# Optimization experiments

Measured on AMD Instinct MI355X. Metric: run time of the kernel, lower is better.

## Reference

```python
import jax, jax.numpy as jnp
import numpy as np

N_VALUES = 10
STRIDE = 2

# sign binarization with straight-through estimator (identity gradient)
@jax.custom_vjp
def binarize(x):
    return jnp.sign(x)

def _bin_fwd(x):
    return jnp.sign(x), None

def _bin_bwd(res, g):
    return (g,)

binarize.defvjp(_bin_fwd, _bin_bwd)


def setup_inputs() -> dict:
    key = jax.random.key(0)
    k1, k2, k3, k4 = jax.random.split(key, 4)
    B, C, H = 16, 1, 28
    D = 2048
    x = jax.random.uniform(k1, (B, C, H, H), dtype=jnp.float32)          # float image in [0,1)
    values = jax.random.normal(k2, (N_VALUES, D), dtype=jnp.float32)     # value-vector embedding table
    w = jax.random.normal(k3, (D, D, 5, 5), dtype=jnp.float32) * 0.05    # binary conv weight (OIHW)
    b = jax.random.normal(k4, (D,), dtype=jnp.float32) * 0.01            # conv bias
    return {"x": x, "values": values, "w": w, "b": b}


def reference(x, values, w, b):
    n = values.shape[0]
    # quantize pixel intensities to value-vector indices (truncation, like .long())
    idx = (x[:, 0] * (n - 1)).astype(jnp.int32)            # [B, H, W]
    # embedding lookup of binarized value vectors
    emb = binarize(values)[idx]                            # [B, H, W, D]
    emb = jnp.transpose(emb, (0, 3, 1, 2))                 # [B, D, H, W]
    # binary-weight conv2d, kernel 5, stride 2, no padding
    out = jax.lax.conv_general_dilated(
        emb, binarize(w),
        window_strides=(STRIDE, STRIDE), padding='VALID',
        dimension_numbers=('NCHW', 'OIHW', 'NCHW'))
    out = out + b[None, :, None, None]                     # [B, D, 12, 12]
    return binarize(out)
```

## Files before the change

### kernel.cpp

```cpp
#include <hip/hip_runtime.h>

#define NV    10
#define DD    2048
#define TAPS  25
#define CHUNK 128
#define NCHH  8
#define NGRP  (DD / 64)
#define HGRP  16
#define OB    64

typedef __attribute__((address_space(1))) const unsigned int gu32;
typedef __attribute__((address_space(3))) unsigned int lu32;

__device__ __forceinline__ float bsign(float v) {
    return (v > 0.0f) ? 1.0f : ((v < 0.0f) ? -1.0f : 0.0f);
}

__global__ __launch_bounds__(64) void vpack_kernel(
        const float* __restrict__ values,
        unsigned long long* __restrict__ vnz,
        unsigned long long* __restrict__ vng) {
    const int b    = blockIdx.x;
    const int n    = b >> 5;
    const int g    = b & 31;
    const int lane = threadIdx.x;
    float f = values[n * DD + g * 64 + lane];
    unsigned long long nz = __ballot(f != 0.0f);
    unsigned long long ng = __ballot(f < 0.0f);
    if (lane == 0) {
        vnz[n * NGRP + g] = nz;
        vng[n * NGRP + g] = ng;
    }
}

__global__ __launch_bounds__(256) void g_kernel(
        const float* __restrict__ w,
        const unsigned long long* __restrict__ gvnz,
        const unsigned long long* __restrict__ gvng,
        float* __restrict__ G) {
    const int bid  = blockIdx.x;
    const int o    = bid >> 1;
    const int half = bid & 1;
    const int t    = threadIdx.x;
    const int lane = t & 63;
    const int wv   = t >> 6;

    __shared__ float ls_raw[CHUNK * TAPS + 32];
    __shared__ unsigned long long s_wnz[2][TAPS * 2];
    __shared__ unsigned long long s_wng[2][TAPS * 2];
    __shared__ unsigned long long s_vnz[NV * HGRP];
    __shared__ unsigned long long s_vng[NV * HGRP];

    const float* wo = w + (size_t)o * (DD * TAPS) + (size_t)half * (1024 * TAPS);

    #define PACK_CHUNK(bi)                                                        \
    {                                                                             \
        _Pragma("unroll")                                                         \
        for (int i = 0; i < 4; ++i) {                                             \
            const int tk = wv + 4 * i;                                            \
            if (tk < 14) {                                                        \
                const int q  = tk >> 1;                                           \
                const int sb = tk & 1;                                            \
                const int t0 = 4 * q;                                             \
                const int ba = (sb * 64 + lane) * TAPS + t0;                      \
                float a0 = ls_raw[ba + 0];                                        \
                float a1 = ls_raw[ba + 1];                                        \
                float a2 = ls_raw[ba + 2];                                        \
                float a3 = ls_raw[ba + 3];                                        \
                unsigned long long z0 = __ballot(a0 != 0.0f);                     \
                unsigned long long g0 = __ballot(a0 <  0.0f);                     \
                unsigned long long z1 = __ballot(a1 != 0.0f);                     \
                unsigned long long g1 = __ballot(a1 <  0.0f);                     \
                unsigned long long z2 = __ballot(a2 != 0.0f);                     \
                unsigned long long g2 = __ballot(a2 <  0.0f);                     \
                unsigned long long z3 = __ballot(a3 != 0.0f);                     \
                unsigned long long g3 = __ballot(a3 <  0.0f);                     \
                if (lane == 0) {                                                  \
                    s_wnz[bi][(t0 + 0) * 2 + sb] = z0;                            \
                    s_wng[bi][(t0 + 0) * 2 + sb] = g0;                            \
                    if (t0 + 1 < TAPS) {                                          \
                        s_wnz[bi][(t0 + 1) * 2 + sb] = z1;                        \
                        s_wng[bi][(t0 + 1) * 2 + sb] = g1;                        \
                        s_wnz[bi][(t0 + 2) * 2 + sb] = z2;                        \
                        s_wng[bi][(t0 + 2) * 2 + sb] = g2;                        \
                        s_wnz[bi][(t0 + 3) * 2 + sb] = z3;                        \
                        s_wng[bi][(t0 + 3) * 2 + sb] = g3;                        \
                    }                                                             \
                }                                                                 \
            }                                                                     \
        }                                                                         \
    }

    for (int e = t; e < (CHUNK * TAPS) / 4; e += 256) {
        __builtin_amdgcn_global_load_lds((gu32*)(wo + 4 * e),
                                         (lu32*)(ls_raw + 4 * (e - lane)), 16, 0, 0);
    }
    if (t < NV * HGRP) {
        const int n  = t >> 4;
        const int gl = t & 15;
        s_vnz[t] = gvnz[n * NGRP + half * HGRP + gl];
        s_vng[t] = gvng[n * NGRP + half * HGRP + gl];
    }
    __syncthreads();
    PACK_CHUNK(0)
    __syncthreads();

    const int tap = t / NV;
    const int n   = t - tap * NV;
    int acc = 0;

    for (int ch = 1; ch <= NCHH; ++ch) {
        if (ch < NCHH) {
            const float* src = wo + (size_t)(ch * CHUNK) * TAPS;
            for (int e = t; e < (CHUNK * TAPS) / 4; e += 256) {
                __builtin_amdgcn_global_load_lds((gu32*)(src + 4 * e),
                                                 (lu32*)(ls_raw + 4 * (e - lane)), 16, 0, 0);
            }
        }
        if (t < NV * TAPS) {
            const int pb = (ch - 1) & 1;
            #pragma unroll
            for (int sub = 0; sub < 2; ++sub) {
                unsigned long long wnz = s_wnz[pb][tap * 2 + sub];
                unsigned long long wng = s_wng[pb][tap * 2 + sub];
                unsigned long long vz  = s_vnz[n * HGRP + (ch - 1) * 2 + sub];
                unsigned long long vg  = s_vng[n * HGRP + (ch - 1) * 2 + sub];
                unsigned long long nzb = wnz & vz;
                acc += (int)__popcll(nzb) - 2 * (int)__popcll((wng ^ vg) & nzb);
            }
        }
        if (ch < NCHH) {
            __syncthreads();
            PACK_CHUNK(ch & 1)
            __syncthreads();
        }
    }
    #undef PACK_CHUNK

    if (t < NV * TAPS) {
        G[((size_t)(half * (TAPS * NV) + tap * NV + n) << 11) + o] = (float)acc;
    }
}

__global__ __launch_bounds__(256) void out_kernel(
        const float* __restrict__ x,
        const float* __restrict__ G,
        const float* __restrict__ bias,
        float* __restrict__ out) {
    const int b     = blockIdx.x >> 5;
    const int oc    = blockIdx.x & 31;
    const int obase = oc * OB;
    const int t     = threadIdx.x;
    const int lane  = t & 63;
    const int oq    = t >> 6;

    __shared__ float s_G[TAPS * NV * 65];
    __shared__ int   s_idx[28 * 28];
    __shared__ float s_bias[OB];

    for (int e = t; e < TAPS * NV * 16; e += 256) {
        const int r  = e >> 4;
        const int li = (e & 15) << 2;
        const float4 va = *(const float4*)(G + ((size_t)r << 11) + obase + li);
        const float4 vb = *(const float4*)(G + ((size_t)(r + TAPS * NV) << 11) + obase + li);
        s_G[r * 65 + li]     = va.x + vb.x;
        s_G[r * 65 + li + 1] = va.y + vb.y;
        s_G[r * 65 + li + 2] = va.z + vb.z;
        s_G[r * 65 + li + 3] = va.w + vb.w;
    }
    for (int e = t; e < 28 * 28; e += 256) {
        s_idx[e] = (int)(x[b * 784 + e] * 9.0f);
    }
    if (t < OB) s_bias[t] = bias[obase + t];
    __syncthreads();

    for (int grp = 0; grp < 3; ++grp) {
        const int pos = grp * 64 + lane;
        if (pos < 144) {
            const int oh = pos / 12;
            const int ow = pos - oh * 12;
            int rr[25];
            #pragma unroll
            for (int kh = 0; kh < 5; ++kh) {
                const int row = (oh * 2 + kh) * 28 + ow * 2;
                #pragma unroll
                for (int kw = 0; kw < 5; ++kw) {
                    const int nn = s_idx[row + kw];
                    rr[kh * 5 + kw] = (kh * 5 + kw) * 650 + nn * 65;
                }
            }
            for (int ol = oq; ol < OB; ol += 4) {
                float acc = 0.0f;
                #pragma unroll
                for (int tp = 0; tp < TAPS; ++tp) {
                    acc += s_G[rr[tp] + ol];
                }
                out[((size_t)(b * DD + obase + ol)) * 144 + pos] = bsign(acc + s_bias[ol]);
            }
        }
    }
}

extern "C" void kernel_launch(void* const* d_in, const int* in_sizes, int n_in,
                              void* d_out, int out_size, void* d_ws, size_t ws_size,
                              hipStream_t stream) {
    const float* x      = (const float*)d_in[0];
    const float* values = (const float*)d_in[1];
    const float* w      = (const float*)d_in[2];
    const float* bias   = (const float*)d_in[3];
    float* out = (float*)d_out;

    unsigned long long* vnz = (unsigned long long*)d_ws;
    unsigned long long* vng = vnz + NV * NGRP;
    float* G = (float*)((char*)d_ws + 8192);

    hipLaunchKernelGGL(vpack_kernel, dim3(NV * NGRP), dim3(64), 0, stream, values, vnz, vng);
    hipLaunchKernelGGL(g_kernel, dim3(2 * DD), dim3(256), 0, stream, w, vnz, vng, G);
    hipLaunchKernelGGL(out_kernel, dim3(16 * (DD / OB)), dim3(256), 0, stream, x, G, bias, out);
}
```

Baseline: 117.2 us.

## Fuse value-bit packing into g_kernel and halve output-channel block size

```diff
diff --git a/kernel.cpp b/kernel.cpp
--- a/kernel.cpp
+++ b/kernel.cpp
@@ -7,7 +7,7 @@
 #define NCHH  8
 #define NGRP  (DD / 64)
 #define HGRP  16
-#define OB    64
+#define OB    32
 
 typedef __attribute__((address_space(1))) const unsigned int gu32;
 typedef __attribute__((address_space(3))) unsigned int lu32;
@@ -16,27 +16,9 @@
     return (v > 0.0f) ? 1.0f : ((v < 0.0f) ? -1.0f : 0.0f);
 }
 
-__global__ __launch_bounds__(64) void vpack_kernel(
+__global__ __launch_bounds__(256) void g_kernel(
         const float* __restrict__ values,
-        unsigned long long* __restrict__ vnz,
-        unsigned long long* __restrict__ vng) {
-    const int b    = blockIdx.x;
-    const int n    = b >> 5;
-    const int g    = b & 31;
-    const int lane = threadIdx.x;
-    float f = values[n * DD + g * 64 + lane];
-    unsigned long long nz = __ballot(f != 0.0f);
-    unsigned long long ng = __ballot(f < 0.0f);
-    if (lane == 0) {
-        vnz[n * NGRP + g] = nz;
-        vng[n * NGRP + g] = ng;
-    }
-}
-
-__global__ __launch_bounds__(256) void g_kernel(
         const float* __restrict__ w,
-        const unsigned long long* __restrict__ gvnz,
-        const unsigned long long* __restrict__ gvng,
         float* __restrict__ G) {
     const int bid  = blockIdx.x;
     const int o    = bid >> 1;
@@ -96,10 +78,24 @@
                                          (lu32*)(ls_raw + 4 * (e - lane)), 16, 0, 0);
     }
     if (t < NV * HGRP) {
-        const int n  = t >> 4;
-        const int gl = t & 15;
-        s_vnz[t] = gvnz[n * NGRP + half * HGRP + gl];
-        s_vng[t] = gvng[n * NGRP + half * HGRP + gl];
+        const int n  = t / HGRP;
+        const int gl = t - n * HGRP;
+        const float4* vp = (const float4*)(values + n * DD + half * 1024 + gl * 64);
+        unsigned long long nz = 0ull, ng = 0ull;
+        #pragma unroll
+        for (int j = 0; j < 16; ++j) {
+            const float4 v = vp[j];
+            if (v.x != 0.0f) nz |= 1ull << (4 * j + 0);
+            if (v.x <  0.0f) ng |= 1ull << (4 * j + 0);
+            if (v.y != 0.0f) nz |= 1ull << (4 * j + 1);
+            if (v.y <  0.0f) ng |= 1ull << (4 * j + 1);
+            if (v.z != 0.0f) nz |= 1ull << (4 * j + 2);
+            if (v.z <  0.0f) ng |= 1ull << (4 * j + 2);
+            if (v.w != 0.0f) nz |= 1ull << (4 * j + 3);
+            if (v.w <  0.0f) ng |= 1ull << (4 * j + 3);
+        }
+        s_vnz[n * HGRP + gl] = nz;
+        s_vng[n * HGRP + gl] = ng;
     }
     __syncthreads();
     PACK_CHUNK(0)
@@ -147,26 +143,26 @@
         const float* __restrict__ G,
         const float* __restrict__ bias,
         float* __restrict__ out) {
-    const int b     = blockIdx.x >> 5;
-    const int oc    = blockIdx.x & 31;
+    const int b     = blockIdx.x >> 6;
+    const int oc    = blockIdx.x & 63;
     const int obase = oc * OB;
     const int t     = threadIdx.x;
     const int lane  = t & 63;
     const int oq    = t >> 6;
 
-    __shared__ float s_G[TAPS * NV * 65];
+    __shared__ float s_G[TAPS * NV * 33];
     __shared__ int   s_idx[28 * 28];
     __shared__ float s_bias[OB];
 
-    for (int e = t; e < TAPS * NV * 16; e += 256) {
-        const int r  = e >> 4;
-        const int li = (e & 15) << 2;
+    for (int e = t; e < TAPS * NV * 8; e += 256) {
+        const int r  = e >> 3;
+        const int li = (e & 7) << 2;
         const float4 va = *(const float4*)(G + ((size_t)r << 11) + obase + li);
         const float4 vb = *(const float4*)(G + ((size_t)(r + TAPS * NV) << 11) + obase + li);
-        s_G[r * 65 + li]     = va.x + vb.x;
-        s_G[r * 65 + li + 1] = va.y + vb.y;
-        s_G[r * 65 + li + 2] = va.z + vb.z;
-        s_G[r * 65 + li + 3] = va.w + vb.w;
+        s_G[r * 33 + li]     = va.x + vb.x;
+        s_G[r * 33 + li + 1] = va.y + vb.y;
+        s_G[r * 33 + li + 2] = va.z + vb.z;
+        s_G[r * 33 + li + 3] = va.w + vb.w;
     }
     for (int e = t; e < 28 * 28; e += 256) {
         s_idx[e] = (int)(x[b * 784 + e] * 9.0f);
@@ -186,7 +182,7 @@
                 #pragma unroll
                 for (int kw = 0; kw < 5; ++kw) {
                     const int nn = s_idx[row + kw];
-                    rr[kh * 5 + kw] = (kh * 5 + kw) * 650 + nn * 65;
+                    rr[kh * 5 + kw] = (kh * 5 + kw) * 330 + nn * 33;
                 }
             }
             for (int ol = oq; ol < OB; ol += 4) {
@@ -209,12 +205,8 @@
     const float* w      = (const float*)d_in[2];
     const float* bias   = (const float*)d_in[3];
     float* out = (float*)d_out;
-
-    unsigned long long* vnz = (unsigned long long*)d_ws;
-    unsigned long long* vng = vnz + NV * NGRP;
-    float* G = (float*)((char*)d_ws + 8192);
-
-    hipLaunchKernelGGL(vpack_kernel, dim3(NV * NGRP), dim3(64), 0, stream, values, vnz, vng);
-    hipLaunchKernelGGL(g_kernel, dim3(2 * DD), dim3(256), 0, stream, w, vnz, vng, G);
+    float* G   = (float*)d_ws;
+
+    hipLaunchKernelGGL(g_kernel, dim3(2 * DD), dim3(256), 0, stream, values, w, G);
     hipLaunchKernelGGL(out_kernel, dim3(16 * (DD / OB)), dim3(256), 0, stream, x, G, bias, out);
 }
```

After: 126.6 us. 8.0% more time.
